# Optimization experiments

Hardware: AMD Instinct MI355X
Metric: run time of the kernel (lower is better)

## Reference

```python
import jax, jax.numpy as jnp
import numpy as np

N_NODES = 100000
N_EDGES = 1600000
D_IN = 128
D_HID = 128


def setup_inputs() -> dict:
    key = jax.random.key(0)
    ks = jax.random.split(key, 8)
    x = jax.random.normal(ks[0], (N_NODES, D_IN), dtype=jnp.float32)
    edge_index = jax.random.randint(ks[1], (2, N_EDGES), 0, N_NODES, dtype=jnp.int64)
    s = 1.0 / np.sqrt(D_IN)
    W_root1 = jax.random.normal(ks[2], (D_IN, D_HID), dtype=jnp.float32) * s
    W_rel1 = jax.random.normal(ks[3], (D_IN, D_HID), dtype=jnp.float32) * s
    b1 = jnp.zeros((D_HID,), dtype=jnp.float32)
    sh = 1.0 / np.sqrt(D_HID)
    W_root2 = jax.random.normal(ks[4], (D_HID, D_HID), dtype=jnp.float32) * sh
    W_rel2 = jax.random.normal(ks[5], (D_HID, D_HID), dtype=jnp.float32) * sh
    b2 = jnp.zeros((D_HID,), dtype=jnp.float32)
    return {"x": x, "edge_index": edge_index, "W_root1": W_root1, "W_rel1": W_rel1,
            "b1": b1, "W_root2": W_root2, "W_rel2": W_rel2, "b2": b2}


def graph_conv(x, src, dst, W_root, W_rel, b):
    # PyG GraphConv: out_i = x_i @ W_root + (sum_{j in N(i)} x_j) @ W_rel + b
    agg = jax.ops.segment_sum(x[src], dst, num_segments=N_NODES)  # [N, d]
    return x @ W_root + agg @ W_rel + b


def reference(x, edge_index, W_root1, W_rel1, b1, W_root2, W_rel2, b2):
    src, dst = edge_index[0], edge_index[1]
    h = jax.nn.relu(graph_conv(x, src, dst, W_root1, W_rel1, b1))
    # dropout is identity in eval mode (reference baseline)
    h = jax.nn.relu(graph_conv(h, src, dst, W_root2, W_rel2, b2))
    return h
```

## Files before the change

### kernel.cpp

```cpp
#include <hip/hip_runtime.h>

#define D 128
#define KTOT 256
#define GM 128
#define LPAD 8
#define LSTR (KTOT + LPAD)

#define EB1   4096
#define BKT_W 64
#define WIN   512
#define EMAX  8192
#define HB1MAX 2048

typedef __attribute__((ext_vector_type(8))) short bf16x8;
typedef __attribute__((ext_vector_type(4))) float f32x4;

__device__ __forceinline__ unsigned short f2b(float f) {
    unsigned int u = __float_as_uint(f);
    u += 0x7fffu + ((u >> 16) & 1u);
    return (unsigned short)(u >> 16);
}
__device__ __forceinline__ float blo(unsigned int u) { return __uint_as_float(u << 16); }
__device__ __forceinline__ float bhi(unsigned int u) { return __uint_as_float(u & 0xffff0000u); }

__global__ void detect_kernel(const unsigned int* __restrict__ ei, int* __restrict__ flag) {
    int all0 = 1;
    for (int i = 0; i < 128; ++i) {
        if (ei[2 * i + 1] != 0u) { all0 = 0; break; }
    }
    *flag = all0;
}

__global__ __launch_bounds__(256) void pack2_kernel(
    const void* __restrict__ ei, const int* __restrict__ flag,
    unsigned int* __restrict__ pk, unsigned short* __restrict__ bkt, int n_edges)
{
    int e = blockIdx.x * 256 + threadIdx.x;
    if (e >= n_edges) return;
    int s, d;
    if (*flag) {
        const long long* p = (const long long*)ei;
        s = (int)p[e]; d = (int)p[n_edges + e];
    } else {
        const int* p = (const int*)ei;
        s = p[e]; d = p[n_edges + e];
    }
    pk[e]  = ((unsigned int)s << 6) | (unsigned int)(d & (BKT_W - 1));
    bkt[e] = (unsigned short)(d >> 6);
}

__global__ __launch_bounds__(256) void s1_count_kernel(
    const unsigned short* __restrict__ bkt, int n_edges, int nb1,
    int* __restrict__ C)
{
    __shared__ int h[HB1MAX];
    for (int i = threadIdx.x; i < nb1; i += 256) h[i] = 0;
    __syncthreads();
    const int e0 = blockIdx.x * EB1;
    const int e1 = min(e0 + EB1, n_edges);
    for (int e = e0 + threadIdx.x; e < e1; e += 256)
        atomicAdd(&h[bkt[e]], 1);
    __syncthreads();
    int* out = C + (long long)blockIdx.x * nb1;
    for (int i = threadIdx.x; i < nb1; i += 256) out[i] = h[i];
}

__global__ __launch_bounds__(1024) void scanA_kernel(
    const int* __restrict__ C, int* __restrict__ Cs,
    int* __restrict__ blockSums, int L, int nb1, int nblk1)
{
    __shared__ int sm[1024];
    const int tid = threadIdx.x;
    const int i = blockIdx.x * 1024 + tid;
    int v = 0;
    if (i < L) {
        int b = i / nblk1, k = i - b * nblk1;
        v = C[(long long)k * nb1 + b];
    }
    int val = v;
    sm[tid] = val;
    __syncthreads();
    for (int off = 1; off < 1024; off <<= 1) {
        int t = (tid >= off) ? sm[tid - off] : 0;
        __syncthreads();
        val += t;
        sm[tid] = val;
        __syncthreads();
    }
    if (i < L) Cs[i] = val - v;
    if (tid == 1023) blockSums[blockIdx.x] = val;
}

__global__ __launch_bounds__(1024) void scan2_kernel(int* __restrict__ bs, int nb)
{
    __shared__ int sm[1024];
    int t = threadIdx.x;
    int v = (t < nb) ? bs[t] : 0;
    int val = v;
    sm[t] = val;
    __syncthreads();
    for (int off = 1; off < 1024; off <<= 1) {
        int u = (t >= off) ? sm[t - off] : 0;
        __syncthreads();
        val += u;
        sm[t] = val;
        __syncthreads();
    }
    if (t < nb) bs[t] = val - v;
}

__global__ __launch_bounds__(1024) void scan3_kernel(
    int* __restrict__ arr, const int* __restrict__ blockSums, int n)
{
    const int i = blockIdx.x * 1024 + threadIdx.x;
    if (i >= n) return;
    arr[i] += blockSums[blockIdx.x];
}

__global__ __launch_bounds__(256) void s1_scatter_kernel(
    const unsigned short* __restrict__ bkt, const unsigned int* __restrict__ pk,
    const int* __restrict__ Cs, unsigned int* __restrict__ sorted,
    int n_edges, int nb1, int nblk1, int lo)
{
    __shared__ int cur[WIN];
    const int hi = min(lo + WIN, nb1);
    for (int t = threadIdx.x; t < hi - lo; t += 256)
        cur[t] = Cs[(long long)(lo + t) * nblk1 + blockIdx.x];
    __syncthreads();
    const int e0 = blockIdx.x * EB1;
    const int e1 = min(e0 + EB1, n_edges);
    for (int e = e0 + threadIdx.x; e < e1; e += 256) {
        int b = bkt[e];
        if (b >= lo && b < hi) {
            int pos = atomicAdd(&cur[b - lo], 1);
            sorted[pos] = pk[e];
        }
    }
}

__global__ __launch_bounds__(256) void bucket_sort_kernel(
    unsigned int* __restrict__ sorted, const int* __restrict__ Cs,
    int n_edges, int n_nodes, int nb1, int nblk1, int* __restrict__ row_end)
{
    __shared__ unsigned int lpk[EMAX];
    __shared__ int h64[BKT_W], excl[BKT_W + 1], cur[BKT_W];
    const int b = blockIdx.x;
    const int t = threadIdx.x;
    const int base = Cs[(long long)b * nblk1];
    const int nextb = (b + 1 < nb1) ? Cs[(long long)(b + 1) * nblk1] : n_edges;
    const int cnt = min(nextb - base, EMAX);

    if (t < BKT_W) h64[t] = 0;
    for (int i = t; i < cnt; i += 256) lpk[i] = sorted[base + i];
    __syncthreads();
    for (int i = t; i < cnt; i += 256) atomicAdd(&h64[lpk[i] & (BKT_W - 1)], 1);
    __syncthreads();
    if (t == 0) {
        int run = 0;
        #pragma unroll
        for (int i = 0; i < BKT_W; ++i) { excl[i] = run; run += h64[i]; }
        excl[BKT_W] = run;
    }
    __syncthreads();
    const int node0 = b * BKT_W;
    const int bins = min(BKT_W, n_nodes - node0);
    if (t < bins) row_end[node0 + t] = base + excl[t + 1];
    if (t < BKT_W) cur[t] = excl[t];
    __syncthreads();
    for (int i = t; i < cnt; i += 256) {
        unsigned int p = lpk[i];
        int pos = atomicAdd(&cur[p & (BKT_W - 1)], 1);
        sorted[base + pos] = p >> 6;
    }
}

__global__ __launch_bounds__(256) void cvt_kernel(
    const float* __restrict__ in, unsigned short* __restrict__ out, long long nelem)
{
    long long i = ((long long)blockIdx.x * 256 + threadIdx.x) * 8;
    if (i >= nelem) return;
    float4 a = *(const float4*)(in + i);
    float4 b = *(const float4*)(in + i + 4);
    bf16x8 v;
    v[0] = (short)f2b(a.x); v[1] = (short)f2b(a.y);
    v[2] = (short)f2b(a.z); v[3] = (short)f2b(a.w);
    v[4] = (short)f2b(b.x); v[5] = (short)f2b(b.y);
    v[6] = (short)f2b(b.z); v[7] = (short)f2b(b.w);
    *(bf16x8*)(out + i) = v;
}

__global__ __launch_bounds__(256) void wt_kernel(
    const float* __restrict__ Wr, const float* __restrict__ Wl,
    unsigned short* __restrict__ Wt)
{
    int c = blockIdx.x, k = threadIdx.x;
    float v = (k < 128) ? Wr[k * D + c] : Wl[(k - 128) * D + c];
    Wt[c * KTOT + k] = f2b(v);
}

__global__ __launch_bounds__(256) void agg_kernel(
    const unsigned short* __restrict__ src, const int* __restrict__ sorted_src,
    const int* __restrict__ row_end, unsigned short* __restrict__ dst, int n)
{
    const int node = blockIdx.x * 4 + (threadIdx.x >> 6);
    if (node >= n) return;
    const int lane = threadIdx.x & 63;
    const int j = lane >> 4;
    const int c = (lane & 15) * 8;
    const int beg = node ? row_end[node - 1] : 0;
    const int end = row_end[node];

    float a0 = 0.f, a1 = 0.f, a2 = 0.f, a3 = 0.f,
          a4 = 0.f, a5 = 0.f, a6 = 0.f, a7 = 0.f;

    int i = beg + j;
    for (; i + 4 < end; i += 8) {
        int s0 = sorted_src[i];
        int s1 = sorted_src[i + 4];
        uint4 u0 = *(const uint4*)(src + (long long)s0 * D + c);
        uint4 u1 = *(const uint4*)(src + (long long)s1 * D + c);
        a0 += blo(u0.x); a1 += bhi(u0.x); a2 += blo(u0.y); a3 += bhi(u0.y);
        a4 += blo(u0.z); a5 += bhi(u0.z); a6 += blo(u0.w); a7 += bhi(u0.w);
        a0 += blo(u1.x); a1 += bhi(u1.x); a2 += blo(u1.y); a3 += bhi(u1.y);
        a4 += blo(u1.z); a5 += bhi(u1.z); a6 += blo(u1.w); a7 += bhi(u1.w);
    }
    if (i < end) {
        int s0 = sorted_src[i];
        uint4 u0 = *(const uint4*)(src + (long long)s0 * D + c);
        a0 += blo(u0.x); a1 += bhi(u0.x); a2 += blo(u0.y); a3 += bhi(u0.y);
        a4 += blo(u0.z); a5 += bhi(u0.z); a6 += blo(u0.w); a7 += bhi(u0.w);
    }

    a0 += __shfl_xor(a0, 16); a1 += __shfl_xor(a1, 16);
    a2 += __shfl_xor(a2, 16); a3 += __shfl_xor(a3, 16);
    a4 += __shfl_xor(a4, 16); a5 += __shfl_xor(a5, 16);
    a6 += __shfl_xor(a6, 16); a7 += __shfl_xor(a7, 16);
    a0 += __shfl_xor(a0, 32); a1 += __shfl_xor(a1, 32);
    a2 += __shfl_xor(a2, 32); a3 += __shfl_xor(a3, 32);
    a4 += __shfl_xor(a4, 32); a5 += __shfl_xor(a5, 32);
    a6 += __shfl_xor(a6, 32); a7 += __shfl_xor(a7, 32);

    if (j == 0) {
        uint4 p;
        p.x = (unsigned int)f2b(a0) | ((unsigned int)f2b(a1) << 16);
        p.y = (unsigned int)f2b(a2) | ((unsigned int)f2b(a3) << 16);
        p.z = (unsigned int)f2b(a4) | ((unsigned int)f2b(a5) << 16);
        p.w = (unsigned int)f2b(a6) | ((unsigned int)f2b(a7) << 16);
        *(uint4*)(dst + (long long)node * D + c) = p;
    }
}

template <int OUT_BF16>
__global__ __launch_bounds__(512) void gemm_kernel(
    const unsigned short* __restrict__ Xop, const unsigned short* __restrict__ Aop,
    const unsigned short* __restrict__ Wt, const float* __restrict__ bias,
    void* outp, int n)
{
    __shared__ short sW[D][LSTR];
    const int tid = threadIdx.x;
    const int r0 = blockIdx.x * GM;

    for (int i = 0; i < 8; ++i) {
        int idx = tid + i * 512;
        int r = idx >> 5, c8 = idx & 31;
        bf16x8 w = *(const bf16x8*)(Wt + r * KTOT + c8 * 8);
        *(bf16x8*)&sW[r][c8 * 8] = w;
    }
    __syncthreads();

    const int w    = tid >> 6;
    const int lane = tid & 63;
    const int lr   = lane & 15;
    const int lk   = (lane >> 4) * 8;
    const int row  = r0 + w * 16 + lr;
    const bool rok = (row < n);

    f32x4 acc[8];
    #pragma unroll
    for (int ct = 0; ct < 8; ++ct) acc[ct] = (f32x4){0.f, 0.f, 0.f, 0.f};

    #pragma unroll
    for (int ks = 0; ks < 8; ++ks) {
        bf16x8 a = {};
        if (rok) {
            const unsigned short* base = (ks < 4) ? Xop : Aop;
            a = *(const bf16x8*)(base + (long long)row * D + (ks & 3) * 32 + lk);
        }
        #pragma unroll
        for (int ct = 0; ct < 8; ++ct) {
            bf16x8 bf = *(const bf16x8*)&sW[ct * 16 + lr][ks * 32 + lk];
            acc[ct] = __builtin_amdgcn_mfma_f32_16x16x32_bf16(a, bf, acc[ct], 0, 0, 0);
        }
    }

    const int rbase = r0 + w * 16 + (lane >> 4) * 4;
    #pragma unroll
    for (int ct = 0; ct < 8; ++ct) {
        const int col = ct * 16 + lr;
        const float bv = bias[col];
        #pragma unroll
        for (int j = 0; j < 4; ++j) {
            int orow = rbase + j;
            if (orow < n) {
                float val = fmaxf(acc[ct][j] + bv, 0.f);
                if (OUT_BF16) {
                    ((unsigned short*)outp)[(long long)orow * D + col] = f2b(val);
                } else {
                    ((float*)outp)[(long long)orow * D + col] = val;
                }
            }
        }
    }
}

static inline size_t align_up(size_t v, size_t a) { return (v + a - 1) & ~(a - 1); }

extern "C" void kernel_launch(void* const* d_in, const int* in_sizes, int n_in,
                              void* d_out, int out_size, void* d_ws, size_t ws_size,
                              hipStream_t stream) {
    const float* x   = (const float*)d_in[0];
    const void*  ei  = d_in[1];
    const float* Wr1 = (const float*)d_in[2];
    const float* Wl1 = (const float*)d_in[3];
    const float* b1  = (const float*)d_in[4];
    const float* Wr2 = (const float*)d_in[5];
    const float* Wl2 = (const float*)d_in[6];
    const float* b2  = (const float*)d_in[7];
    float* out = (float*)d_out;

    const int n_nodes = in_sizes[0] / D;
    const int n_edges = in_sizes[1] / 2;

    const int nb1   = (n_nodes + BKT_W - 1) / BKT_W;
    const int nblk1 = (n_edges + EB1 - 1) / EB1;
    const int L     = nb1 * nblk1;
    const int npass = (nb1 + WIN - 1) / WIN;
    const int nbL   = (L + 1023) / 1024;

    char* ws = (char*)d_ws;
    size_t off_flag = 0;
    size_t off_rs   = 256;
    size_t off_bs   = align_up(off_rs + 4 * (size_t)(n_nodes + 1), 256);
    size_t off_ssrc = align_up(off_bs + 4 * 1024, 256);
    size_t off_wt   = align_up(off_ssrc + 4 * (size_t)n_edges, 256);
    size_t off_xb   = align_up(off_wt + 2 * (size_t)D * KTOT, 256);
    size_t off_ab   = align_up(off_xb + 2 * (size_t)n_nodes * D, 256);

    int* flag            = (int*)(ws + off_flag);
    int* row_end         = (int*)(ws + off_rs);
    int* blockSums       = (int*)(ws + off_bs);
    unsigned int* sorted = (unsigned int*)(ws + off_ssrc);
    unsigned short* Wt   = (unsigned short*)(ws + off_wt);
    unsigned short* Xb   = (unsigned short*)(ws + off_xb);
    unsigned short* Ab   = (unsigned short*)(ws + off_ab);
    unsigned int*   pk  = (unsigned int*)(ws + off_xb);
    unsigned short* bkt = (unsigned short*)(pk + n_edges);
    int* C  = (int*)(ws + off_ab);
    int* Cs = C + L;

    const int edge_blocks = (n_edges + 255) / 256;
    const int gemm_blocks = (n_nodes + GM - 1) / GM;
    const int agg_blocks  = (n_nodes + 3) / 4;
    const long long nfeat = (long long)n_nodes * D;

    detect_kernel<<<1, 1, 0, stream>>>((const unsigned int*)ei, flag);

    pack2_kernel<<<edge_blocks, 256, 0, stream>>>(ei, flag, pk, bkt, n_edges);
    s1_count_kernel<<<nblk1, 256, 0, stream>>>(bkt, n_edges, nb1, C);
    scanA_kernel<<<nbL, 1024, 0, stream>>>(C, Cs, blockSums, L, nb1, nblk1);
    scan2_kernel<<<1, 1024, 0, stream>>>(blockSums, nbL);
    scan3_kernel<<<nbL, 1024, 0, stream>>>(Cs, blockSums, L);
    for (int p = 0; p < npass; ++p) {
        s1_scatter_kernel<<<nblk1, 256, 0, stream>>>(
            bkt, pk, Cs, sorted, n_edges, nb1, nblk1, p * WIN);
    }
    bucket_sort_kernel<<<nb1, 256, 0, stream>>>(
        sorted, Cs, n_edges, n_nodes, nb1, nblk1, row_end);

    cvt_kernel<<<(int)((nfeat / 8 + 255) / 256), 256, 0, stream>>>(x, Xb, nfeat);
    wt_kernel<<<D, KTOT, 0, stream>>>(Wr1, Wl1, Wt);

    agg_kernel<<<agg_blocks, 256, 0, stream>>>(Xb, (const int*)sorted, row_end, Ab, n_nodes);
    gemm_kernel<1><<<gemm_blocks, 512, 0, stream>>>(Xb, Ab, Wt, b1, Ab, n_nodes);

    wt_kernel<<<D, KTOT, 0, stream>>>(Wr2, Wl2, Wt);
    agg_kernel<<<agg_blocks, 256, 0, stream>>>(Ab, (const int*)sorted, row_end, Xb, n_nodes);
    gemm_kernel<0><<<gemm_blocks, 512, 0, stream>>>(Ab, Xb, Wt, b2, out, n_nodes);
}
```

Measured before the change: 269.6 us.

## Fuse setup kernels, inline int64 detection, deepen gather unroll, enlarge sort tiles

Removes the single-thread detect kernel by having every pack2 wave check the index width itself with a wave vote. The x conversion and both weight transposes are merged into one prep kernel, with separate buffers for the two weight sets. The aggregation loop is unrolled to four outstanding gathers per lane. The edge block size and scatter window are doubled, which halves the scatter passes. Together these cut kernel launches and serial latency and add memory-level parallelism, at the cost of more registers and larger shared histograms.

```diff
diff --git a/kernel.cpp b/kernel.cpp
--- a/kernel.cpp
+++ b/kernel.cpp
@@ -6,9 +6,9 @@
 #define LPAD 8
 #define LSTR (KTOT + LPAD)
 
-#define EB1   4096
+#define EB1   8192
 #define BKT_W 64
-#define WIN   512
+#define WIN   1024
 #define EMAX  8192
 #define HB1MAX 2048
 
@@ -23,22 +23,20 @@
 __device__ __forceinline__ float blo(unsigned int u) { return __uint_as_float(u << 16); }
 __device__ __forceinline__ float bhi(unsigned int u) { return __uint_as_float(u & 0xffff0000u); }
 
-__global__ void detect_kernel(const unsigned int* __restrict__ ei, int* __restrict__ flag) {
-    int all0 = 1;
-    for (int i = 0; i < 128; ++i) {
-        if (ei[2 * i + 1] != 0u) { all0 = 0; break; }
-    }
-    *flag = all0;
-}
-
 __global__ __launch_bounds__(256) void pack2_kernel(
-    const void* __restrict__ ei, const int* __restrict__ flag,
-    unsigned int* __restrict__ pk, unsigned short* __restrict__ bkt, int n_edges)
-{
+    const void* __restrict__ ei, unsigned int* __restrict__ pk,
+    unsigned short* __restrict__ bkt, int n_edges)
+{
+    const unsigned int* eiu = (const unsigned int*)ei;
+    const int l = threadIdx.x & 63;
+    unsigned int w0 = eiu[2 * l + 1];
+    unsigned int w1 = eiu[2 * (l + 64) + 1];
+    const int is64 = __all((w0 | w1) == 0u);
+
     int e = blockIdx.x * 256 + threadIdx.x;
     if (e >= n_edges) return;
     int s, d;
-    if (*flag) {
+    if (is64) {
         const long long* p = (const long long*)ei;
         s = (int)p[e]; d = (int)p[n_edges + e];
     } else {
@@ -174,29 +172,40 @@
     }
 }
 
-__global__ __launch_bounds__(256) void cvt_kernel(
-    const float* __restrict__ in, unsigned short* __restrict__ out, long long nelem)
-{
-    long long i = ((long long)blockIdx.x * 256 + threadIdx.x) * 8;
-    if (i >= nelem) return;
-    float4 a = *(const float4*)(in + i);
-    float4 b = *(const float4*)(in + i + 4);
-    bf16x8 v;
-    v[0] = (short)f2b(a.x); v[1] = (short)f2b(a.y);
-    v[2] = (short)f2b(a.z); v[3] = (short)f2b(a.w);
-    v[4] = (short)f2b(b.x); v[5] = (short)f2b(b.y);
-    v[6] = (short)f2b(b.z); v[7] = (short)f2b(b.w);
-    *(bf16x8*)(out + i) = v;
-}
-
-__global__ __launch_bounds__(256) void wt_kernel(
-    const float* __restrict__ Wr, const float* __restrict__ Wl,
-    unsigned short* __restrict__ Wt)
-{
-    int c = blockIdx.x, k = threadIdx.x;
-    float v = (k < 128) ? Wr[k * D + c] : Wl[(k - 128) * D + c];
-    Wt[c * KTOT + k] = f2b(v);
-}
+__global__ __launch_bounds__(256) void prep_kernel(
+    const float* __restrict__ x, unsigned short* __restrict__ Xb,
+    long long nelem, int nbcvt,
+    const float* __restrict__ Wr1, const float* __restrict__ Wl1,
+    unsigned short* __restrict__ Wt1,
+    const float* __restrict__ Wr2, const float* __restrict__ Wl2,
+    unsigned short* __restrict__ Wt2)
+{
+    const int b = blockIdx.x;
+    if (b < nbcvt) {
+        long long i = ((long long)b * 256 + threadIdx.x) * 8;
+        if (i >= nelem) return;
+        float4 a = *(const float4*)(x + i);
+        float4 c = *(const float4*)(x + i + 4);
+        bf16x8 v;
+        v[0] = (short)f2b(a.x); v[1] = (short)f2b(a.y);
+        v[2] = (short)f2b(a.z); v[3] = (short)f2b(a.w);
+        v[4] = (short)f2b(c.x); v[5] = (short)f2b(c.y);
+        v[6] = (short)f2b(c.z); v[7] = (short)f2b(c.w);
+        *(bf16x8*)(Xb + i) = v;
+    } else {
+        const int cb = b - nbcvt;
+        const float* Wr = (cb < 128) ? Wr1 : Wr2;
+        const float* Wl = (cb < 128) ? Wl1 : Wl2;
+        unsigned short* Wt = (cb < 128) ? Wt1 : Wt2;
+        const int c = cb & 127;
+        const int k = threadIdx.x;
+        float v = (k < 128) ? Wr[k * D + c] : Wl[(k - 128) * D + c];
+        Wt[c * KTOT + k] = f2b(v);
+    }
+}
+
+#define ACC8(u) { a0 += blo(u.x); a1 += bhi(u.x); a2 += blo(u.y); a3 += bhi(u.y); \
+                  a4 += blo(u.z); a5 += bhi(u.z); a6 += blo(u.w); a7 += bhi(u.w); }
 
 __global__ __launch_bounds__(256) void agg_kernel(
     const unsigned short* __restrict__ src, const int* __restrict__ sorted_src,
@@ -214,21 +223,21 @@
           a4 = 0.f, a5 = 0.f, a6 = 0.f, a7 = 0.f;
 
     int i = beg + j;
-    for (; i + 4 < end; i += 8) {
+    for (; i + 12 < end; i += 16) {
         int s0 = sorted_src[i];
         int s1 = sorted_src[i + 4];
+        int s2 = sorted_src[i + 8];
+        int s3 = sorted_src[i + 12];
         uint4 u0 = *(const uint4*)(src + (long long)s0 * D + c);
         uint4 u1 = *(const uint4*)(src + (long long)s1 * D + c);
-        a0 += blo(u0.x); a1 += bhi(u0.x); a2 += blo(u0.y); a3 += bhi(u0.y);
-        a4 += blo(u0.z); a5 += bhi(u0.z); a6 += blo(u0.w); a7 += bhi(u0.w);
-        a0 += blo(u1.x); a1 += bhi(u1.x); a2 += blo(u1.y); a3 += bhi(u1.y);
-        a4 += blo(u1.z); a5 += bhi(u1.z); a6 += blo(u1.w); a7 += bhi(u1.w);
-    }
-    if (i < end) {
+        uint4 u2 = *(const uint4*)(src + (long long)s2 * D + c);
+        uint4 u3 = *(const uint4*)(src + (long long)s3 * D + c);
+        ACC8(u0); ACC8(u1); ACC8(u2); ACC8(u3);
+    }
+    for (; i < end; i += 4) {
         int s0 = sorted_src[i];
         uint4 u0 = *(const uint4*)(src + (long long)s0 * D + c);
-        a0 += blo(u0.x); a1 += bhi(u0.x); a2 += blo(u0.y); a3 += bhi(u0.y);
-        a4 += blo(u0.z); a5 += bhi(u0.z); a6 += blo(u0.w); a7 += bhi(u0.w);
+        ACC8(u0);
     }
 
     a0 += __shfl_xor(a0, 16); a1 += __shfl_xor(a1, 16);
@@ -338,19 +347,19 @@
     const int nbL   = (L + 1023) / 1024;
 
     char* ws = (char*)d_ws;
-    size_t off_flag = 0;
-    size_t off_rs   = 256;
+    size_t off_rs   = 0;
     size_t off_bs   = align_up(off_rs + 4 * (size_t)(n_nodes + 1), 256);
     size_t off_ssrc = align_up(off_bs + 4 * 1024, 256);
-    size_t off_wt   = align_up(off_ssrc + 4 * (size_t)n_edges, 256);
-    size_t off_xb   = align_up(off_wt + 2 * (size_t)D * KTOT, 256);
+    size_t off_wt1  = align_up(off_ssrc + 4 * (size_t)n_edges, 256);
+    size_t off_wt2  = align_up(off_wt1 + 2 * (size_t)D * KTOT, 256);
+    size_t off_xb   = align_up(off_wt2 + 2 * (size_t)D * KTOT, 256);
     size_t off_ab   = align_up(off_xb + 2 * (size_t)n_nodes * D, 256);
 
-    int* flag            = (int*)(ws + off_flag);
     int* row_end         = (int*)(ws + off_rs);
     int* blockSums       = (int*)(ws + off_bs);
     unsigned int* sorted = (unsigned int*)(ws + off_ssrc);
-    unsigned short* Wt   = (unsigned short*)(ws + off_wt);
+    unsigned short* Wt1  = (unsigned short*)(ws + off_wt1);
+    unsigned short* Wt2  = (unsigned short*)(ws + off_wt2);
     unsigned short* Xb   = (unsigned short*)(ws + off_xb);
     unsigned short* Ab   = (unsigned short*)(ws + off_ab);
     unsigned int*   pk  = (unsigned int*)(ws + off_xb);
@@ -362,10 +371,9 @@
     const int gemm_blocks = (n_nodes + GM - 1) / GM;
     const int agg_blocks  = (n_nodes + 3) / 4;
     const long long nfeat = (long long)n_nodes * D;
-
-    detect_kernel<<<1, 1, 0, stream>>>((const unsigned int*)ei, flag);
-
-    pack2_kernel<<<edge_blocks, 256, 0, stream>>>(ei, flag, pk, bkt, n_edges);
+    const int nbcvt = (int)((nfeat / 8 + 255) / 256);
+
+    pack2_kernel<<<edge_blocks, 256, 0, stream>>>(ei, pk, bkt, n_edges);
     s1_count_kernel<<<nblk1, 256, 0, stream>>>(bkt, n_edges, nb1, C);
     scanA_kernel<<<nbL, 1024, 0, stream>>>(C, Cs, blockSums, L, nb1, nblk1);
     scan2_kernel<<<1, 1024, 0, stream>>>(blockSums, nbL);
@@ -374,16 +382,16 @@
         s1_scatter_kernel<<<nblk1, 256, 0, stream>>>(
             bkt, pk, Cs, sorted, n_edges, nb1, nblk1, p * WIN);
     }
+
+    prep_kernel<<<nbcvt + 256, 256, 0, stream>>>(
+        x, Xb, nfeat, nbcvt, Wr1, Wl1, Wt1, Wr2, Wl2, Wt2);
+
     bucket_sort_kernel<<<nb1, 256, 0, stream>>>(
         sorted, Cs, n_edges, n_nodes, nb1, nblk1, row_end);
 
-    cvt_kernel<<<(int)((nfeat / 8 + 255) / 256), 256, 0, stream>>>(x, Xb, nfeat);
-    wt_kernel<<<D, KTOT, 0, stream>>>(Wr1, Wl1, Wt);
-
     agg_kernel<<<agg_blocks, 256, 0, stream>>>(Xb, (const int*)sorted, row_end, Ab, n_nodes);
-    gemm_kernel<1><<<gemm_blocks, 512, 0, stream>>>(Xb, Ab, Wt, b1, Ab, n_nodes);
-
-    wt_kernel<<<D, KTOT, 0, stream>>>(Wr2, Wl2, Wt);
+    gemm_kernel<1><<<gemm_blocks, 512, 0, stream>>>(Xb, Ab, Wt1, b1, Ab, n_nodes);
+
     agg_kernel<<<agg_blocks, 256, 0, stream>>>(Ab, (const int*)sorted, row_end, Xb, n_nodes);
-    gemm_kernel<0><<<gemm_blocks, 512, 0, stream>>>(Ab, Xb, Wt, b2, out, n_nodes);
-}
+    gemm_kernel<0><<<gemm_blocks, 512, 0, stream>>>(Ab, Xb, Wt2, b2, out, n_nodes);
+}
```

Result: faster. 260.5 us (-3.4%).
